# Kernel optimization log

Hardware: AMD Instinct MI355X
Metric: run time of the kernel (lower is better)

## Reference

```python
import jax, jax.numpy as jnp
import numpy as np

MODS = ['linguistic', 'emotient', 'acoustic', 'image']
HID = {'linguistic': 128, 'emotient': 20, 'acoustic': 64, 'image': 128}
DIMS = {'linguistic': 300, 'emotient': 30, 'acoustic': 88, 'image': 1000}
B, T = 64, 512
TOTAL_HID = sum(HID[m] for m in MODS)  # 340
FUSE_HID = 64


def setup_inputs() -> dict:
    key = jax.random.key(0)
    ks = iter(jax.random.split(key, 64))
    inp = {}
    for mod in MODS:
        H, D = HID[mod], DIMS[mod]
        s = 1.0 / np.sqrt(H)
        inp[f'x_{mod}'] = jax.random.normal(next(ks), (B, T, D), jnp.float32)
        inp[f'present_{mod}'] = jax.random.randint(next(ks), (B, T), 0, 2).astype(jnp.int32)
        inp[f'W_ih_{mod}'] = jax.random.uniform(next(ks), (4 * H, D), jnp.float32, -s, s)
        inp[f'W_hh_{mod}'] = jax.random.uniform(next(ks), (4 * H, H), jnp.float32, -s, s)
        inp[f'b_ih_{mod}'] = jax.random.uniform(next(ks), (4 * H,), jnp.float32, -s, s)
        inp[f'b_hh_{mod}'] = jax.random.uniform(next(ks), (4 * H,), jnp.float32, -s, s)
    inp['seq_length'] = jax.random.randint(next(ks), (B,), 1, T + 1).astype(jnp.int32)
    valid = (jnp.arange(T)[None, :] < inp['seq_length'][:, None])
    inp['lstm_masks'] = valid.astype(jnp.float32)[:, :, None]
    s1 = 1.0 / np.sqrt(TOTAL_HID)
    inp['fuse_W1'] = jax.random.uniform(next(ks), (FUSE_HID, TOTAL_HID), jnp.float32, -s1, s1)
    inp['fuse_b1'] = jax.random.uniform(next(ks), (FUSE_HID,), jnp.float32, -s1, s1)
    s2 = 1.0 / np.sqrt(FUSE_HID)
    inp['fuse_W2'] = jax.random.uniform(next(ks), (1, FUSE_HID), jnp.float32, -s2, s2)
    inp['fuse_b2'] = jax.random.uniform(next(ks), (1,), jnp.float32, -s2, s2)
    return inp


def _lstm_scan(x, present, W_ih, W_hh, b_ih, b_hh):
    # x: [B,T,D], present: [B,T] in {0,1}. Carries (h,c) when not present (async arrival).
    Bn, Tn, _ = x.shape
    H = W_hh.shape[1]
    xg = jnp.einsum('btd,gd->btg', x, W_ih) + b_ih  # [B,T,4H] batched input GEMM

    def step(carry, inp):
        h, c = carry
        xg_t, p_t = inp  # [B,4H], [B]
        g = xg_t + h @ W_hh.T + b_hh
        i, f, gg, o = jnp.split(g, 4, axis=-1)
        i, f, o = jax.nn.sigmoid(i), jax.nn.sigmoid(f), jax.nn.sigmoid(o)
        gg = jnp.tanh(gg)
        c_new = f * c + i * gg
        h_new = o * jnp.tanh(c_new)
        p = p_t[:, None].astype(h.dtype)
        h2 = p * h_new + (1.0 - p) * h
        c2 = p * c_new + (1.0 - p) * c
        return (h2, c2), h2

    init = (jnp.zeros((Bn, H), x.dtype), jnp.zeros((Bn, H), x.dtype))
    _, hs = jax.lax.scan(step, init, (jnp.swapaxes(xg, 0, 1), present.T))
    return jnp.swapaxes(hs, 0, 1)  # [B,T,H]


def reference(x_linguistic, x_emotient, x_acoustic, x_image,
              present_linguistic, present_emotient, present_acoustic, present_image,
              W_ih_linguistic, W_hh_linguistic, b_ih_linguistic, b_hh_linguistic,
              W_ih_emotient, W_hh_emotient, b_ih_emotient, b_hh_emotient,
              W_ih_acoustic, W_hh_acoustic, b_ih_acoustic, b_hh_acoustic,
              W_ih_image, W_hh_image, b_ih_image, b_hh_image,
              seq_length, lstm_masks, fuse_W1, fuse_b1, fuse_W2, fuse_b2):
    xs = {'linguistic': x_linguistic, 'emotient': x_emotient, 'acoustic': x_acoustic, 'image': x_image}
    pres = {'linguistic': present_linguistic, 'emotient': present_emotient,
            'acoustic': present_acoustic, 'image': present_image}
    Wih = {'linguistic': W_ih_linguistic, 'emotient': W_ih_emotient, 'acoustic': W_ih_acoustic, 'image': W_ih_image}
    Whh = {'linguistic': W_hh_linguistic, 'emotient': W_hh_emotient, 'acoustic': W_hh_acoustic, 'image': W_hh_image}
    bih = {'linguistic': b_ih_linguistic, 'emotient': b_ih_emotient, 'acoustic': b_ih_acoustic, 'image': b_ih_image}
    bhh = {'linguistic': b_hh_linguistic, 'emotient': b_hh_emotient, 'acoustic': b_hh_acoustic, 'image': b_hh_image}
    hs = [_lstm_scan(xs[m], pres[m], Wih[m], Whh[m], bih[m], bhh[m]) for m in MODS]
    h = jnp.concatenate(hs, axis=-1)  # [B,T,340]
    # padded timesteps past seq_length are zeros in the original (zeros appended)
    valid = (jnp.arange(h.shape[1])[None, :] < seq_length[:, None]).astype(h.dtype)
    h = h * valid[:, :, None]
    out = h @ fuse_W1.T + fuse_b1  # Dropout is identity at inference
    out = out @ fuse_W2.T + fuse_b2
    return out * lstm_masks
```

## Files before the change

kernel.cpp:

```cpp
#include <hip/hip_runtime.h>
#include <stdint.h>

typedef __bf16 bf16_t;
typedef _Float16 fp16_t;
typedef bf16_t bf16x8 __attribute__((ext_vector_type(8)));
typedef fp16_t fp16x4 __attribute__((ext_vector_type(4)));
typedef float f32x4 __attribute__((ext_vector_type(4)));

#define LOG2E 1.44269504088896340736f

__device__ __forceinline__ float sigm(float x) {
    return __builtin_amdgcn_rcpf(1.f + __builtin_amdgcn_exp2f(-LOG2E * x));
}
__device__ __forceinline__ float tanh_(float x) {
    return 1.f - 2.f * __builtin_amdgcn_rcpf(1.f + __builtin_amdgcn_exp2f((2.f * LOG2E) * x));
}

template <int CTRL>
__device__ __forceinline__ float dpp_add(float x) {
    int perm = __builtin_amdgcn_update_dpp(0, __float_as_int(x), CTRL, 0xF, 0xF, true);
    return x + __int_as_float(perm);
}
__device__ __forceinline__ float red16(float x) {
    x = dpp_add<0xB1>(x);
    x = dpp_add<0x4E>(x);
    x = dpp_add<0x124>(x);
    x = dpp_add<0x128>(x);
    return x;
}

__device__ __forceinline__ void gate_chunk(const int* fp, int need, int tid) {
    if ((tid >> 6) == 0) {
        while (__hip_atomic_load(fp, __ATOMIC_RELAXED, __HIP_MEMORY_SCOPE_AGENT) < need)
            __builtin_amdgcn_s_sleep(2);
        (void)__hip_atomic_load(fp, __ATOMIC_ACQUIRE, __HIP_MEMORY_SCOPE_AGENT);
    }
    __syncthreads();
}

__global__ void prep_fuse(const float* __restrict__ W1, const float* __restrict__ b1,
                          const float* __restrict__ W2, const float* __restrict__ b2,
                          float* __restrict__ v) {
    int u = threadIdx.x;
    if (u < 340) {
        float s = 0.f;
        for (int j = 0; j < 64; j++) s += W2[j] * W1[j * 340 + u];
        v[u] = s;
    } else if (u == 340) {
        float s = 0.f;
        for (int j = 0; j < 64; j++) s += W2[j] * b1[j];
        v[340] = s + b2[0];
    }
}

struct ModGemm {
    const float* x; const float* w; const float* bih; const float* bhh; fp16_t* xg;
    int D; int KB; int N4; int hshift;
};
struct ModRec {
    const float* whh; const int* present; const fp16_t* xg;
    int N4; int voff;
};
struct MegaArgs {
    ModGemm gm[4];
    int slot_mi[11]; int slot_nb[11];
    ModRec rm[4];
    const float* vvec;
    float* s_out;
    int* flags;
    int need[4];
};

__device__ void gemm_body(const ModGemm mg, int nb, int bm, int mi,
                          int* __restrict__ flags, int tid,
                          bf16_t* sAh, bf16_t* sAl, bf16_t* sB) {
    const int ncol0 = nb << 7;
    const int w = tid >> 6, l = tid & 63, lm = l & 15, q = l >> 4;
    const int wm = w & 3, wn = w >> 2;
    const int D = mg.D, N4 = mg.N4;
    const int ra = tid >> 1, ca = (tid & 1) << 4;
    const int rb = tid >> 2, cb = (tid & 3) << 3;

    f32x4 acc[4][4];
#pragma unroll
    for (int a = 0; a < 4; a++)
#pragma unroll
        for (int b = 0; b < 4; b++) acc[a][b] = 0.f;

    for (int kb = 0; kb < mg.KB; kb++) {
        const int k0 = kb << 5;
        {
            long row = (long)(bm << 8) + ra;
            int tt = (int)(row >> 6), bb = (int)(row & 63);
            const float* base = mg.x + ((size_t)bb * 512 + tt) * D;
            const float* src = base + k0 + ca;
            union { bf16_t e[16]; bf16x8 v[2]; } uh, ul;
            if (k0 + ca + 16 <= D) {
#pragma unroll
                for (int j = 0; j < 16; j += 2) {
                    float2 f = *(const float2*)(src + j);
                    bf16_t h0 = (bf16_t)f.x, h1 = (bf16_t)f.y;
                    uh.e[j] = h0; uh.e[j + 1] = h1;
                    ul.e[j] = (bf16_t)(f.x - (float)h0);
                    ul.e[j + 1] = (bf16_t)(f.y - (float)h1);
                }
            } else {
#pragma unroll
                for (int j = 0; j < 16; j++) {
                    int k = k0 + ca + j;
                    float fv = (k < D) ? base[k] : 0.f;
                    bf16_t h0 = (bf16_t)fv;
                    uh.e[j] = h0; ul.e[j] = (bf16_t)(fv - (float)h0);
                }
            }
            *(bf16x8*)&sAh[ra * 40 + ca] = uh.v[0];
            *(bf16x8*)&sAh[ra * 40 + ca + 8] = uh.v[1];
            *(bf16x8*)&sAl[ra * 40 + ca] = ul.v[0];
            *(bf16x8*)&sAl[ra * 40 + ca + 8] = ul.v[1];
        }
        {
            int wrow = ncol0 + rb;
            bool vr = wrow < N4;
            const float* src = mg.w + (long)wrow * D + k0 + cb;
            union { bf16_t e[8]; bf16x8 v; } ub;
            if (vr && (k0 + cb + 8 <= D)) {
#pragma unroll
                for (int j = 0; j < 8; j += 2) {
                    float2 f = *(const float2*)(src + j);
                    ub.e[j] = (bf16_t)f.x; ub.e[j + 1] = (bf16_t)f.y;
                }
            } else {
#pragma unroll
                for (int j = 0; j < 8; j++) {
                    int k = k0 + cb + j;
                    ub.e[j] = (vr && k < D) ? (bf16_t)mg.w[(long)wrow * D + k] : (bf16_t)0.f;
                }
            }
            *(bf16x8*)&sB[rb * 40 + cb] = ub.v;
        }
        __syncthreads();
        bf16x8 ah[4], al[4];
#pragma unroll
        for (int mt = 0; mt < 4; mt++) {
            int row = (wm << 6) + (mt << 4) + lm;
            ah[mt] = *(const bf16x8*)&sAh[row * 40 + (q << 3)];
            al[mt] = *(const bf16x8*)&sAl[row * 40 + (q << 3)];
        }
#pragma unroll
        for (int nt = 0; nt < 4; nt++) {
            bf16x8 bfv = *(const bf16x8*)&sB[((wn << 6) + (nt << 4) + lm) * 40 + (q << 3)];
#pragma unroll
            for (int mt = 0; mt < 4; mt++) {
                acc[mt][nt] = __builtin_amdgcn_mfma_f32_16x16x32_bf16(ah[mt], bfv, acc[mt][nt], 0, 0, 0);
                acc[mt][nt] = __builtin_amdgcn_mfma_f32_16x16x32_bf16(al[mt], bfv, acc[mt][nt], 0, 0, 0);
            }
        }
        __syncthreads();
    }
#pragma unroll
    for (int nt = 0; nt < 4; nt++) {
        int col = ncol0 + (wn << 6) + (nt << 4) + lm;
        if (col >= N4) continue;
        float bias = mg.bih[col] + mg.bhh[col];
        int colout = mg.hshift ? ((col & ((1 << mg.hshift) - 1)) << 2) | (col >> mg.hshift) : col;
#pragma unroll
        for (int mt = 0; mt < 4; mt++) {
#pragma unroll
            for (int r = 0; r < 4; r++) {
                long row = (long)(bm << 8) + (wm << 6) + (mt << 4) + (q << 2) + r;
                mg.xg[(size_t)row * N4 + colout] = (fp16_t)(acc[mt][nt][r] + bias);
            }
        }
    }
    __syncthreads();
    if (tid == 0) {
        __threadfence();
        __hip_atomic_fetch_add(&flags[mi * 128 + bm], 1, __ATOMIC_RELEASE,
                               __HIP_MEMORY_SCOPE_AGENT);
    }
}

template <int H>
__device__ __forceinline__ void rec_step(
    int t, bool act, int w, int lm, int q, int b0,
    const bf16x8 (&wf)[4][H / 32], float vv,
    fp16x4 (&xvs)[4], const fp16_t* const (&px)[4], size_t tstride,
    float (&h_st)[4], float (&c_st)[4],
    const unsigned (&pw)[4], const bf16_t* __restrict__ hbR,
    bf16_t* __restrict__ hbW, float* __restrict__ s_out) {
    constexpr int KT = H / 32, Hp = H + 8;
    if (act) {
        bf16x8 af[KT];
#pragma unroll
        for (int kt = 0; kt < KT; kt++)
            af[kt] = *(const bf16x8*)&hbR[lm * Hp + (kt << 5) + (q << 3)];
        f32x4 accv[4];
#pragma unroll
        for (int g = 0; g < 4; g++)
#pragma unroll
            for (int r = 0; r < 4; r++)
                accv[g][r] = (float)xvs[r][g];
        int tn = t + 4;
        if (tn < 512) {
#pragma unroll
            for (int r = 0; r < 4; r++)
                xvs[r] = *(const fp16x4*)(px[r] + (size_t)tn * tstride);
        }
#pragma unroll
        for (int kt = 0; kt < KT; kt++)
#pragma unroll
            for (int g = 0; g < 4; g++)
                accv[g] = __builtin_amdgcn_mfma_f32_16x16x32_bf16(af[kt], wf[g][kt], accv[g], 0, 0, 0);
        float cr[4];
#pragma unroll
        for (int r = 0; r < 4; r++) {
            float gi = sigm(accv[0][r]);
            float gf = sigm(accv[1][r]);
            float gg = tanh_(accv[2][r]);
            float go = sigm(accv[3][r]);
            float cn = gf * c_st[r] + gi * gg;
            float hn = go * tanh_(cn);
            bool pb = ((pw[r] >> (t & 31)) & 1u) != 0u;
            h_st[r] = pb ? hn : h_st[r];
            c_st[r] = pb ? cn : c_st[r];
            cr[r] = h_st[r] * vv;
        }
        const int u = (w << 4) + lm;
#pragma unroll
        for (int r = 0; r < 4; r++)
            hbW[((q << 2) + r) * Hp + u] = (bf16_t)h_st[r];
#pragma unroll
        for (int r = 0; r < 4; r++)
            cr[r] = red16(cr[r]);
        if (lm == 0) {
#pragma unroll
            for (int r = 0; r < 4; r++)
                s_out[(size_t)((w << 6) + b0 + (q << 2) + r) * 512 + t] = cr[r];
        }
    }
    __syncthreads();
}

template <int H>
__device__ void rec_mfma(const ModRec M, int grp, float* __restrict__ s_out,
                         const float* __restrict__ vvec,
                         const int* __restrict__ flagp, int need,
                         unsigned* presw, bf16_t* hb0, bf16_t* hb1, int tid) {
    constexpr int KT = H / 32, TPG = H / 16, Hp = H + 8;
    const int N4 = 4 * H;
    const int w = tid >> 6, l = tid & 63, lm = l & 15, q = l >> 4;
    const int b0 = grp << 4;
    const bool act = (w < TPG);

    for (int i = tid; i < 16 * Hp; i += 512) { hb0[i] = (bf16_t)0.f; hb1[i] = (bf16_t)0.f; }
    for (int i = tid; i < 256; i += 512) {
        const int* ps = M.present + ((b0 + (i >> 4)) << 9) + ((i & 15) << 5);
        unsigned bits = 0u;
#pragma unroll
        for (int j = 0; j < 32; j++) bits |= (unsigned)(ps[j] != 0) << j;
        presw[i] = bits;
    }

    bf16x8 wf[4][KT];
    float vv = 0.f;
    const int u = (w << 4) + lm;
    if (act) {
#pragma unroll
        for (int g = 0; g < 4; g++) {
            int n = g * H + u;
#pragma unroll
            for (int kt = 0; kt < KT; kt++) {
                int k = (kt << 5) + (q << 3);
                const float* sp_ = M.whh + (long)n * H + k;
                float4 f0 = *(const float4*)sp_;
                float4 f1 = *(const float4*)(sp_ + 4);
                union { bf16_t e[8]; bf16x8 v; } uu;
                uu.e[0] = (bf16_t)f0.x; uu.e[1] = (bf16_t)f0.y;
                uu.e[2] = (bf16_t)f0.z; uu.e[3] = (bf16_t)f0.w;
                uu.e[4] = (bf16_t)f1.x; uu.e[5] = (bf16_t)f1.y;
                uu.e[6] = (bf16_t)f1.z; uu.e[7] = (bf16_t)f1.w;
                wf[g][kt] = uu.v;
            }
        }
        vv = vvec[M.voff + u];
    }
    const fp16_t* px[4];
#pragma unroll
    for (int r = 0; r < 4; r++)
        px[r] = M.xg + (size_t)(b0 + (q << 2) + r) * N4 + (u << 2);
    const size_t tstride = (size_t)64 * N4;

    gate_chunk(flagp, need, tid);

    fp16x4 xv[4][4];
    if (act) {
#pragma unroll
        for (int s = 0; s < 4; s++)
#pragma unroll
            for (int r = 0; r < 4; r++)
                xv[s][r] = *(const fp16x4*)(px[r] + (size_t)s * tstride);
    }
    float h_st[4] = {0, 0, 0, 0}, c_st[4] = {0, 0, 0, 0};
    unsigned pw[4] = {0, 0, 0, 0};
    __syncthreads();

    for (int t0 = 0; t0 < 512; t0 += 4) {
        int cn = (t0 >> 2) + 1;
        if (cn < 128) gate_chunk(flagp + cn, need, tid);
        if ((t0 & 31) == 0 && act) {
            int wd = t0 >> 5;
#pragma unroll
            for (int r = 0; r < 4; r++)
                pw[r] = presw[(((q << 2) + r) << 4) + wd];
        }
        rec_step<H>(t0 + 0, act, w, lm, q, b0, wf, vv, xv[0], px, tstride, h_st, c_st, pw, hb0, hb1, s_out);
        rec_step<H>(t0 + 1, act, w, lm, q, b0, wf, vv, xv[1], px, tstride, h_st, c_st, pw, hb1, hb0, s_out);
        rec_step<H>(t0 + 2, act, w, lm, q, b0, wf, vv, xv[2], px, tstride, h_st, c_st, pw, hb0, hb1, s_out);
        rec_step<H>(t0 + 3, act, w, lm, q, b0, wf, vv, xv[3], px, tstride, h_st, c_st, pw, hb1, hb0, s_out);
    }
}

__device__ void rec_emot(const ModRec M, int grp, float* __restrict__ s_out,
                         const float* __restrict__ vvec,
                         const int* __restrict__ flagp, int need,
                         float* presf, float* gbuf , float* he , int tid) {
    const int b0 = grp << 4;
    for (int i = tid; i < 16 * 21; i += 512) he[i] = 0.f;
    for (int i = tid; i < 16 * 512; i += 512)
        presf[i] = (float)M.present[((b0 + (i >> 9)) << 9) + (i & 511)];
    const int bl = tid >> 5;
    const int j0 = tid & 31;
    const bool has2 = (j0 < 16);
    float wr0[20], wr1[20], wr2[20];
#pragma unroll
    for (int k = 0; k < 20; k++) {
        wr0[k] = M.whh[j0 * 20 + k];
        wr1[k] = M.whh[(j0 + 32) * 20 + k];
        wr2[k] = has2 ? M.whh[(j0 + 64) * 20 + k] : 0.f;
    }
    const int b2 = tid / 20, u2 = tid % 20;
    const bool p2 = (tid < 320);
    float c_st = 0.f, h_st = 0.f;
    const fp16_t* px = M.xg + (size_t)(b0 + bl) * 80;

    gate_chunk(flagp, need, tid);

    fp16_t e0[4], e1[4], e2[4];
#pragma unroll
    for (int s = 0; s < 4; s++) {
        const fp16_t* p = px + (size_t)s * 5120;
        e0[s] = p[j0]; e1[s] = p[j0 + 32]; e2[s] = has2 ? p[j0 + 64] : (fp16_t)0.f;
    }
    __syncthreads();

    for (int t0 = 0; t0 < 512; t0 += 4) {
        int cn = (t0 >> 2) + 1;
        if (cn < 128) gate_chunk(flagp + cn, need, tid);
#pragma unroll
        for (int s = 0; s < 4; s++) {
            int t = t0 + s;
            float g0 = (float)e0[s];
            float g1 = (float)e1[s];
            float g2 = has2 ? (float)e2[s] : 0.f;
            int tn = t + 4;
            if (tn < 512) {
                const fp16_t* p = px + (size_t)tn * 5120;
                e0[s] = p[j0]; e1[s] = p[j0 + 32]; if (has2) e2[s] = p[j0 + 64];
            }
#pragma unroll
            for (int k = 0; k < 20; k++) {
                float hv = he[bl * 21 + k];
                g0 += wr0[k] * hv; g1 += wr1[k] * hv; g2 += wr2[k] * hv;
            }
            gbuf[bl * 81 + j0] = g0;
            gbuf[bl * 81 + j0 + 32] = g1;
            if (has2) gbuf[bl * 81 + j0 + 64] = g2;
            __syncthreads();
            if (p2) {
                float gi = sigm(gbuf[b2 * 81 + u2]);
                float gf = sigm(gbuf[b2 * 81 + u2 + 20]);
                float gg = tanh_(gbuf[b2 * 81 + u2 + 40]);
                float go = sigm(gbuf[b2 * 81 + u2 + 60]);
                float cn2 = gf * c_st + gi * gg;
                float hn = go * tanh_(cn2);
                float p = presf[b2 * 512 + t];
                bool pb = (p != 0.f);
                h_st = pb ? hn : h_st;
                c_st = pb ? cn2 : c_st;
                he[b2 * 21 + u2] = h_st;
            }
            __syncthreads();
            if (tid < 16) {
                float ssum = 0.f;
#pragma unroll
                for (int uu = 0; uu < 20; uu++) ssum += he[tid * 21 + uu] * vvec[M.voff + uu];
                s_out[((b0 + tid) << 9) + t] = ssum;
            }
        }
    }
}

__global__ __launch_bounds__(512) void mega(MegaArgs A) {
    __shared__ __align__(16) char smem[51712];
    const int tid = threadIdx.x;
    const int bid = blockIdx.x;
    if (bid < 16) {
        float*    presf = (float*)smem;
        bf16_t*   hb0   = (bf16_t*)(smem + 32768);
        bf16_t*   hb1   = (bf16_t*)(smem + 37120);
        float*    gbuf  = (float*)(smem + 41472);
        float*    he    = (float*)(smem + 46656);
        unsigned* presw = (unsigned*)(smem + 48000);
        const int mi = bid >> 2, grp = bid & 3;
        const ModRec M = A.rm[mi];
        const int* flagp = A.flags + mi * 128;
        const int need = A.need[mi];
        float* s_out = A.s_out + (size_t)mi * 8 * 64 * 512;
        if (mi == 1)      rec_emot(M, grp, s_out, A.vvec, flagp, need, presf, gbuf, he, tid);
        else if (mi == 2) rec_mfma<64>(M, grp, s_out, A.vvec, flagp, need, presw, hb0, hb1, tid);
        else              rec_mfma<128>(M, grp, s_out, A.vvec, flagp, need, presw, hb0, hb1, tid);
    } else {
        bf16_t* sAh = (bf16_t*)smem;
        bf16_t* sAl = (bf16_t*)(smem + 20480);
        bf16_t* sB  = (bf16_t*)(smem + 40960);
        int e = bid - 16;
        int bmi = e / 11;
        int slot = e - bmi * 11;
        int mi = A.slot_mi[slot];
        gemm_body(A.gm[mi], A.slot_nb[slot], bmi, mi, A.flags, tid, sAh, sAl, sB);
    }
}

__global__ void fuse_out(const float* __restrict__ sp, const float* __restrict__ v,
                         const float* __restrict__ masks, float* __restrict__ out) {
    int i = threadIdx.x + blockIdx.x * 256;
    float c0 = v[340];
    float s = 0.f;
#pragma unroll
    for (int w = 0; w < 8; w++) s += sp[(size_t)w * 32768 + i];
    s += sp[(size_t)8 * 32768 + i];
#pragma unroll
    for (int w = 16; w < 20; w++) s += sp[(size_t)w * 32768 + i];
#pragma unroll
    for (int w = 24; w < 32; w++) s += sp[(size_t)w * 32768 + i];
    out[i] = masks[i] * (s + c0);
}

extern "C" void kernel_launch(void* const* d_in, const int* in_sizes, int n_in,
                              void* d_out, int out_size, void* d_ws, size_t ws_size,
                              hipStream_t stream) {
    const float* xL = (const float*)d_in[0];
    const int*   pL = (const int*)d_in[1];
    const float* WihL = (const float*)d_in[2];
    const float* WhhL = (const float*)d_in[3];
    const float* bihL = (const float*)d_in[4];
    const float* bhhL = (const float*)d_in[5];
    const float* xE = (const float*)d_in[6];
    const int*   pE = (const int*)d_in[7];
    const float* WihE = (const float*)d_in[8];
    const float* WhhE = (const float*)d_in[9];
    const float* bihE = (const float*)d_in[10];
    const float* bhhE = (const float*)d_in[11];
    const float* xA = (const float*)d_in[12];
    const int*   pA = (const int*)d_in[13];
    const float* WihA = (const float*)d_in[14];
    const float* WhhA = (const float*)d_in[15];
    const float* bihA = (const float*)d_in[16];
    const float* bhhA = (const float*)d_in[17];
    const float* xI = (const float*)d_in[18];
    const int*   pI = (const int*)d_in[19];
    const float* WihI = (const float*)d_in[20];
    const float* WhhI = (const float*)d_in[21];
    const float* bihI = (const float*)d_in[22];
    const float* bhhI = (const float*)d_in[23];
    const float* masks = (const float*)d_in[25];
    const float* fW1 = (const float*)d_in[26];
    const float* fb1 = (const float*)d_in[27];
    const float* fW2 = (const float*)d_in[28];
    const float* fb2 = (const float*)d_in[29];

    char* ws = (char*)d_ws;
    float* v     = (float*)ws;
    int*   flags = (int*)(ws + 4096);
    float* spart = (float*)(ws + (1 << 16));
    fp16_t* xgL = (fp16_t*)(ws + (1 << 16) + (4 << 20));
    fp16_t* xgE = xgL + (size_t)32768 * 512;
    fp16_t* xgA = xgE + (size_t)32768 * 80;
    fp16_t* xgI = xgA + (size_t)32768 * 256;

    prep_fuse<<<dim3(1), dim3(512), 0, stream>>>(fW1, fb1, fW2, fb2, v);
    hipMemsetAsync(flags, 0, 4 * 128 * sizeof(int), stream);

    MegaArgs A;
    A.gm[0] = {xL, WihL, bihL, bhhL, xgL, 300,  10, 512, 7};
    A.gm[1] = {xE, WihE, bihE, bhhE, xgE, 30,   1,  80,  0};
    A.gm[2] = {xA, WihA, bihA, bhhA, xgA, 88,   3,  256, 6};
    A.gm[3] = {xI, WihI, bihI, bhhI, xgI, 1000, 32, 512, 7};
    const int mi_tab[11] = {0, 0, 0, 0, 3, 3, 3, 3, 2, 2, 1};
    const int nb_tab[11] = {0, 1, 2, 3, 0, 1, 2, 3, 0, 1, 0};
    for (int i = 0; i < 11; i++) { A.slot_mi[i] = mi_tab[i]; A.slot_nb[i] = nb_tab[i]; }
    A.rm[0] = {WhhL, pL, xgL, 512, 0};
    A.rm[1] = {WhhE, pE, xgE, 80,  128};
    A.rm[2] = {WhhA, pA, xgA, 256, 148};
    A.rm[3] = {WhhI, pI, xgI, 512, 212};
    A.vvec = v;
    A.s_out = spart;
    A.flags = flags;
    A.need[0] = 4; A.need[1] = 1; A.need[2] = 2; A.need[3] = 4;

    mega<<<dim3(16 + 128 * 11), dim3(512), 0, stream>>>(A);

    fuse_out<<<dim3(128), dim3(256), 0, stream>>>(spart, v, masks, (float*)d_out);
}
```

Baseline: 1.030 ms.

## Batch producer-flag waits with lookahead watermark and use coherent loads in recurrences

```diff
diff --git a/kernel.cpp b/kernel.cpp
--- a/kernel.cpp
+++ b/kernel.cpp
@@ -29,13 +29,30 @@
     return x;
 }
 
-__device__ __forceinline__ void gate_chunk(const int* fp, int need, int tid) {
-    if ((tid >> 6) == 0) {
-        while (__hip_atomic_load(fp, __ATOMIC_RELAXED, __HIP_MEMORY_SCOPE_AGENT) < need)
+__device__ __forceinline__ fp16x4 ldg_coh8(const fp16_t* p) {
+    unsigned long long v = __hip_atomic_load((const unsigned long long*)p,
+                                             __ATOMIC_RELAXED, __HIP_MEMORY_SCOPE_AGENT);
+    union { unsigned long long u; fp16x4 f; } c; c.u = v; return c.f;
+}
+__device__ __forceinline__ fp16_t ldg_coh2(const fp16_t* p) {
+    unsigned short v = __hip_atomic_load((const unsigned short*)p,
+                                         __ATOMIC_RELAXED, __HIP_MEMORY_SCOPE_AGENT);
+    union { unsigned short u; fp16_t f; } c; c.u = v; return c.f;
+}
+
+__device__ __forceinline__ void gate_chunk(const int* fp, int need, int cn,
+                                           int tid, int* wml, int& wmr) {
+    if (cn < wmr) return;
+    if (tid == 0) {
+        while (__hip_atomic_load(fp + cn, __ATOMIC_RELAXED, __HIP_MEMORY_SCOPE_AGENT) < need)
             __builtin_amdgcn_s_sleep(2);
-        (void)__hip_atomic_load(fp, __ATOMIC_ACQUIRE, __HIP_MEMORY_SCOPE_AGENT);
+        int ah = cn + 16; if (ah > 127) ah = 127;
+        int nw = (__hip_atomic_load(fp + ah, __ATOMIC_RELAXED, __HIP_MEMORY_SCOPE_AGENT) >= need)
+                     ? ah + 1 : cn + 1;
+        *wml = nw;
     }
     __syncthreads();
+    wmr = *wml;
 }
 
 __global__ void prep_fuse(const float* __restrict__ W1, const float* __restrict__ b1,
@@ -174,7 +191,6 @@
     }
     __syncthreads();
     if (tid == 0) {
-        __threadfence();
         __hip_atomic_fetch_add(&flags[mi * 128 + bm], 1, __ATOMIC_RELEASE,
                                __HIP_MEMORY_SCOPE_AGENT);
     }
@@ -204,7 +220,7 @@
         if (tn < 512) {
 #pragma unroll
             for (int r = 0; r < 4; r++)
-                xvs[r] = *(const fp16x4*)(px[r] + (size_t)tn * tstride);
+                xvs[r] = ldg_coh8(px[r] + (size_t)tn * tstride);
         }
 #pragma unroll
         for (int kt = 0; kt < KT; kt++)
@@ -245,7 +261,7 @@
 __device__ void rec_mfma(const ModRec M, int grp, float* __restrict__ s_out,
                          const float* __restrict__ vvec,
                          const int* __restrict__ flagp, int need,
-                         unsigned* presw, bf16_t* hb0, bf16_t* hb1, int tid) {
+                         unsigned* presw, bf16_t* hb0, bf16_t* hb1, int* wml, int tid) {
     constexpr int KT = H / 32, TPG = H / 16, Hp = H + 8;
     const int N4 = 4 * H;
     const int w = tid >> 6, l = tid & 63, lm = l & 15, q = l >> 4;
@@ -290,7 +306,8 @@
         px[r] = M.xg + (size_t)(b0 + (q << 2) + r) * N4 + (u << 2);
     const size_t tstride = (size_t)64 * N4;
 
-    gate_chunk(flagp, need, tid);
+    int wmr = 0;
+    gate_chunk(flagp, need, 0, tid, wml, wmr);
 
     fp16x4 xv[4][4];
     if (act) {
@@ -298,7 +315,7 @@
         for (int s = 0; s < 4; s++)
 #pragma unroll
             for (int r = 0; r < 4; r++)
-                xv[s][r] = *(const fp16x4*)(px[r] + (size_t)s * tstride);
+                xv[s][r] = ldg_coh8(px[r] + (size_t)s * tstride);
     }
     float h_st[4] = {0, 0, 0, 0}, c_st[4] = {0, 0, 0, 0};
     unsigned pw[4] = {0, 0, 0, 0};
@@ -306,7 +323,7 @@
 
     for (int t0 = 0; t0 < 512; t0 += 4) {
         int cn = (t0 >> 2) + 1;
-        if (cn < 128) gate_chunk(flagp + cn, need, tid);
+        if (cn < 128) gate_chunk(flagp, need, cn, tid, wml, wmr);
         if ((t0 & 31) == 0 && act) {
             int wd = t0 >> 5;
 #pragma unroll
@@ -323,7 +340,8 @@
 __device__ void rec_emot(const ModRec M, int grp, float* __restrict__ s_out,
                          const float* __restrict__ vvec,
                          const int* __restrict__ flagp, int need,
-                         float* presf, float* gbuf , float* he , int tid) {
+                         float* presf, float* gbuf , float* he ,
+                         int* wml, int tid) {
     const int b0 = grp << 4;
     for (int i = tid; i < 16 * 21; i += 512) he[i] = 0.f;
     for (int i = tid; i < 16 * 512; i += 512)
@@ -343,19 +361,22 @@
     float c_st = 0.f, h_st = 0.f;
     const fp16_t* px = M.xg + (size_t)(b0 + bl) * 80;
 
-    gate_chunk(flagp, need, tid);
+    int wmr = 0;
+    gate_chunk(flagp, need, 0, tid, wml, wmr);
 
     fp16_t e0[4], e1[4], e2[4];
 #pragma unroll
     for (int s = 0; s < 4; s++) {
         const fp16_t* p = px + (size_t)s * 5120;
-        e0[s] = p[j0]; e1[s] = p[j0 + 32]; e2[s] = has2 ? p[j0 + 64] : (fp16_t)0.f;
+        e0[s] = ldg_coh2(p + j0);
+        e1[s] = ldg_coh2(p + j0 + 32);
+        e2[s] = has2 ? ldg_coh2(p + j0 + 64) : (fp16_t)0.f;
     }
     __syncthreads();
 
     for (int t0 = 0; t0 < 512; t0 += 4) {
         int cn = (t0 >> 2) + 1;
-        if (cn < 128) gate_chunk(flagp + cn, need, tid);
+        if (cn < 128) gate_chunk(flagp, need, cn, tid, wml, wmr);
 #pragma unroll
         for (int s = 0; s < 4; s++) {
             int t = t0 + s;
@@ -365,7 +386,9 @@
             int tn = t + 4;
             if (tn < 512) {
                 const fp16_t* p = px + (size_t)tn * 5120;
-                e0[s] = p[j0]; e1[s] = p[j0 + 32]; if (has2) e2[s] = p[j0 + 64];
+                e0[s] = ldg_coh2(p + j0);
+                e1[s] = ldg_coh2(p + j0 + 32);
+                if (has2) e2[s] = ldg_coh2(p + j0 + 64);
             }
 #pragma unroll
             for (int k = 0; k < 20; k++) {
@@ -405,20 +428,22 @@
     const int tid = threadIdx.x;
     const int bid = blockIdx.x;
     if (bid < 16) {
+        __builtin_amdgcn_s_setprio(3);
         float*    presf = (float*)smem;
         bf16_t*   hb0   = (bf16_t*)(smem + 32768);
         bf16_t*   hb1   = (bf16_t*)(smem + 37120);
         float*    gbuf  = (float*)(smem + 41472);
         float*    he    = (float*)(smem + 46656);
         unsigned* presw = (unsigned*)(smem + 48000);
+        int*      wml   = (int*)(smem + 49024);
         const int mi = bid >> 2, grp = bid & 3;
         const ModRec M = A.rm[mi];
         const int* flagp = A.flags + mi * 128;
         const int need = A.need[mi];
         float* s_out = A.s_out + (size_t)mi * 8 * 64 * 512;
-        if (mi == 1)      rec_emot(M, grp, s_out, A.vvec, flagp, need, presf, gbuf, he, tid);
-        else if (mi == 2) rec_mfma<64>(M, grp, s_out, A.vvec, flagp, need, presw, hb0, hb1, tid);
-        else              rec_mfma<128>(M, grp, s_out, A.vvec, flagp, need, presw, hb0, hb1, tid);
+        if (mi == 1)      rec_emot(M, grp, s_out, A.vvec, flagp, need, presf, gbuf, he, wml, tid);
+        else if (mi == 2) rec_mfma<64>(M, grp, s_out, A.vvec, flagp, need, presw, hb0, hb1, wml, tid);
+        else              rec_mfma<128>(M, grp, s_out, A.vvec, flagp, need, presw, hb0, hb1, wml, tid);
     } else {
         bf16_t* sAh = (bf16_t*)smem;
         bf16_t* sAl = (bf16_t*)(smem + 20480);
```

Measured after the change: 987.4 us. 1.04x faster.
